# Optimization experiments

Hardware: AMD Instinct MI355X
Metric: run time of the kernel (lower is better)

## Reference

```python
import jax, jax.numpy as jnp
import numpy as np

B, L, O, K, H = 8192, 128, 512, 8, 20  # batch, num_latent, num_obs, causes/node, hidden


def setup_inputs() -> dict:
    key = jax.random.key(0)
    ks = jax.random.split(key, 7)
    x = jax.random.normal(ks[0], (B, L), dtype=jnp.float32)
    # noise ~ Normal(0, 0.1), one scalar per (sample, observed node); noise_coeff = 1.0
    noise = 0.1 * jax.random.normal(ks[1], (B, O), dtype=jnp.float32)
    # latent-cause indices per observed node (fixed in-degree K)
    cause_idx = jax.random.randint(ks[2], (O, K), 0, L, dtype=jnp.int32)
    # per-node MLP weights: Linear(K+1,H) -> tanh -> Linear(H,H) -> tanh -> Linear(H,1)
    W1 = jax.random.normal(ks[3], (O, K + 1, H), dtype=jnp.float32) / np.sqrt(K + 1).astype(np.float32)
    b1 = jnp.zeros((O, H), dtype=jnp.float32)
    W2 = jax.random.normal(ks[4], (O, H, H), dtype=jnp.float32) / np.sqrt(H).astype(np.float32)
    b2 = jnp.zeros((O, H), dtype=jnp.float32)
    W3 = jax.random.normal(ks[5], (O, H), dtype=jnp.float32) / np.sqrt(H).astype(np.float32)
    b3 = jnp.zeros((O,), dtype=jnp.float32)
    return {"x": x, "noise": noise, "cause_idx": cause_idx,
            "W1": W1, "b1": b1, "W2": W2, "b2": b2, "W3": W3, "b3": b3}


def reference(x, noise, cause_idx, W1, b1, W2, b2, W3, b3):
    # Gather each observed node's latent causes: [B, O, K]
    gathered = x[:, cause_idx]
    # Prepend the noise column (torch.cat((noise, x_subset), axis=1)): [B, O, K+1]
    inp = jnp.concatenate([noise[..., None], gathered], axis=-1)
    # Per-node tiny MLP as grouped batched GEMMs
    h = jnp.tanh(jnp.einsum('boi,oih->boh', inp, W1) + b1)   # [B, O, H]
    h = jnp.tanh(jnp.einsum('boh,ohg->bog', h, W2) + b2)     # [B, O, H]
    out = jnp.einsum('boh,oh->bo', h, W3) + b3               # [B, O] (concat of per-node outputs)
    return out
```

## Files before the change

kernel.cpp:

```cpp
#include <hip/hip_runtime.h>

#define B_TOT 8192
#define O_DIM 512
#define L_DIM 128
#define K_DIM 8
#define H_DIM 20

#define TB 64
#define G  16
#define NW 4
#define NTH 256
#define XSTR 65
#define NSTR 17

__device__ __forceinline__ float fast_tanh(float x) {
    float e = __builtin_amdgcn_exp2f(x * 2.885390081777927f);
    float r = __builtin_amdgcn_rcpf(1.0f + e);
    return 1.0f - 2.0f * r;
}

__global__ __launch_bounds__(NTH, 4) void medil_fused(
    const float* __restrict__ x, const float* __restrict__ noise,
    const int* __restrict__ cause_idx,
    const float* __restrict__ W1, const float* __restrict__ b1,
    const float* __restrict__ W2, const float* __restrict__ b2,
    const float* __restrict__ W3, const float* __restrict__ b3,
    float* __restrict__ out)
{
    __shared__ float xT[L_DIM * XSTR];
    __shared__ float nt[TB * NSTR];

    const int tid = threadIdx.x;
    const int o0 = (blockIdx.x & 31) * G;
    const int b0 = (blockIdx.x >> 5) * TB;

    {
        const float4* xg = (const float4*)(x + (size_t)b0 * L_DIM);
        #pragma unroll
        for (int i = 0; i < 8; ++i) {
            int idx = tid + NTH * i;
            int r = idx >> 5, c4 = idx & 31;
            float4 v = xg[r * 32 + c4];
            xT[(c4 * 4 + 0) * XSTR + r] = v.x;
            xT[(c4 * 4 + 1) * XSTR + r] = v.y;
            xT[(c4 * 4 + 2) * XSTR + r] = v.z;
            xT[(c4 * 4 + 3) * XSTR + r] = v.w;
        }
    }
    {
        int r = tid >> 2, c4 = tid & 3;
        float4 v = *(const float4*)(noise + (size_t)(b0 + r) * O_DIM + o0 + c4 * 4);
        nt[r * NSTR + c4 * 4 + 0] = v.x;
        nt[r * NSTR + c4 * 4 + 1] = v.y;
        nt[r * NSTR + c4 * 4 + 2] = v.z;
        nt[r * NSTR + c4 * 4 + 3] = v.w;
    }
    __syncthreads();

    const int lane = tid & 63;
    const int wv = tid >> 6;

    #pragma unroll
    for (int it = 0; it < G / NW; ++it) {
        const int ol = __builtin_amdgcn_readfirstlane(wv * (G / NW) + it);
        const int o  = o0 + ol;

        const float* w1p = W1 + (size_t)o * (K_DIM + 1) * H_DIM;
        const float* b1p = b1 + (size_t)o * H_DIM;
        const float* w2p = W2 + (size_t)o * H_DIM * H_DIM;
        const float* b2p = b2 + (size_t)o * H_DIM;
        const float* w3p = W3 + (size_t)o * H_DIM;
        const int*   cip = cause_idx + (size_t)o * K_DIM;

        float xi[K_DIM];
        #pragma unroll
        for (int k = 0; k < K_DIM; ++k)
            xi[k] = xT[cip[k] * XSTR + lane];
        float inp0 = nt[lane * NSTR + ol];

        float a1[H_DIM];
        #pragma unroll
        for (int h = 0; h < H_DIM; ++h)
            a1[h] = fmaf(inp0, w1p[h], b1p[h]);
        #pragma unroll
        for (int k = 0; k < K_DIM; ++k)
            #pragma unroll
            for (int h = 0; h < H_DIM; ++h)
                a1[h] = fmaf(xi[k], w1p[(k + 1) * H_DIM + h], a1[h]);
        #pragma unroll
        for (int h = 0; h < H_DIM; ++h) a1[h] = fast_tanh(a1[h]);

        float a2[H_DIM];
        #pragma unroll
        for (int g = 0; g < H_DIM; ++g) a2[g] = b2p[g];
        #pragma unroll
        for (int h = 0; h < H_DIM; ++h)
            #pragma unroll
            for (int g = 0; g < H_DIM; ++g)
                a2[g] = fmaf(a1[h], w2p[h * H_DIM + g], a2[g]);
        #pragma unroll
        for (int g = 0; g < H_DIM; ++g) a2[g] = fast_tanh(a2[g]);

        float r = b3[o];
        #pragma unroll
        for (int h = 0; h < H_DIM; ++h) r = fmaf(a2[h], w3p[h], r);
        out[(size_t)(b0 + lane) * O_DIM + o] = r;
    }
}

extern "C" void kernel_launch(void* const* d_in, const int* in_sizes, int n_in,
                              void* d_out, int out_size, void* d_ws, size_t ws_size,
                              hipStream_t stream) {
    const float* x         = (const float*)d_in[0];
    const float* noise     = (const float*)d_in[1];
    const int*   cause_idx = (const int*)d_in[2];
    const float* W1        = (const float*)d_in[3];
    const float* b1        = (const float*)d_in[4];
    const float* W2        = (const float*)d_in[5];
    const float* b2        = (const float*)d_in[6];
    const float* W3        = (const float*)d_in[7];
    const float* b3        = (const float*)d_in[8];
    float* out = (float*)d_out;

    dim3 grid((B_TOT / TB) * (O_DIM / G));
    dim3 block(NTH);
    hipLaunchKernelGGL(medil_fused, grid, block, 0, stream,
                       x, noise, cause_idx, W1, b1, W2, b2, W3, b3, out);
}
```

Baseline: 192.3 us.

## Use bf16 MFMA for hidden layer with smem-staged weights and bf16 latents

Replaces the per-lane scalar 20x20 second-layer GEMV with bf16 16x16x32 MFMA instructions. W2 is transposed and stored as bf16 in shared memory, W1 and the biases are staged in shared memory, and x is stored in shared memory as bf16 with an XOR swizzle. The tile becomes 8 output nodes per block, with each wave computing 8 hidden units per lane across four 16-row batch subtiles and reducing through shuffles. This aims to cut the FMA-bound VALU work and the global weight loads. The cost is bf16 rounding of the inputs and hidden activations, plus extra shared memory and lower occupancy.

```diff
diff --git a/kernel.cpp b/kernel.cpp
--- a/kernel.cpp
+++ b/kernel.cpp
@@ -1,4 +1,5 @@
 #include <hip/hip_runtime.h>
+#include <hip/hip_bf16.h>
 
 #define B_TOT 8192
 #define O_DIM 512
@@ -7,19 +8,31 @@
 #define H_DIM 20
 
 #define TB 64
-#define G  16
-#define NW 4
+#define TO 8
 #define NTH 256
-#define XSTR 65
-#define NSTR 17
+#define XPITCH 66
+
+typedef short bf16x8 __attribute__((ext_vector_type(8)));
+typedef float f32x4  __attribute__((ext_vector_type(4)));
+
+#define OFF_W2T 0
+#define OFF_W1  20480
+#define OFF_BB  29696
+#define OFF_NS  32768
+#define OFF_XT  35072
+#define SMEM_BYTES 51968
 
 __device__ __forceinline__ float fast_tanh(float x) {
     float e = __builtin_amdgcn_exp2f(x * 2.885390081777927f);
     float r = __builtin_amdgcn_rcpf(1.0f + e);
     return 1.0f - 2.0f * r;
 }
-
-__global__ __launch_bounds__(NTH, 4) void medil_fused(
+__device__ __forceinline__ unsigned short f2bf(float f) {
+    unsigned u = __float_as_uint(f);
+    return (unsigned short)((u + 0x8000u) >> 16);
+}
+
+__global__ __launch_bounds__(NTH, 3) void medil_fused(
     const float* __restrict__ x, const float* __restrict__ noise,
     const int* __restrict__ cause_idx,
     const float* __restrict__ W1, const float* __restrict__ b1,
@@ -27,84 +40,152 @@
     const float* __restrict__ W3, const float* __restrict__ b3,
     float* __restrict__ out)
 {
-    __shared__ float xT[L_DIM * XSTR];
-    __shared__ float nt[TB * NSTR];
+    __shared__ __align__(16) char smem[SMEM_BYTES];
+    unsigned short* w2t = (unsigned short*)(smem + OFF_W2T);
+    float*          w1s = (float*)(smem + OFF_W1);
+    float*          bbs = (float*)(smem + OFF_BB);
+    float*          nss = (float*)(smem + OFF_NS);
+    unsigned short* xts = (unsigned short*)(smem + OFF_XT);
 
     const int tid = threadIdx.x;
-    const int o0 = (blockIdx.x & 31) * G;
-    const int b0 = (blockIdx.x >> 5) * TB;
-
-    {
-        const float4* xg = (const float4*)(x + (size_t)b0 * L_DIM);
+    const int o0 = (blockIdx.x & 63) * TO;
+    const int b0 = (blockIdx.x >> 6) * TB;
+
+    {
+        const int ol = tid >> 5, idx = tid & 31;
+        unsigned int* w2z = (unsigned int*)(w2t + ol * 1280);
+        #pragma unroll
+        for (int z = 0; z < 20; ++z) w2z[idx + 32 * z] = 0u;
+        float* w1o = w1s + ol * 288;
+        #pragma unroll
+        for (int z = 0; z < 9; ++z) w1o[idx + 32 * z] = 0.f;
+        float* bbo = bbs + ol * 96;
+        #pragma unroll
+        for (int z = 0; z < 3; ++z) bbo[idx + 32 * z] = 0.f;
+    }
+    __syncthreads();
+    {
+        const int ol = tid >> 5, idx = tid & 31;
+        const int o = o0 + ol;
+        if (idx < 20) {
+            unsigned short* w2o = w2t + ol * 1280;
+            #pragma unroll
+            for (int hi = 0; hi < 20; ++hi)
+                w2o[idx * 40 + hi] = f2bf(W2[(size_t)o * 400 + hi * 20 + idx]);
+            float* w1o = w1s + ol * 288;
+            #pragma unroll
+            for (int k = 0; k < 9; ++k)
+                w1o[k * 32 + idx] = W1[(size_t)o * 180 + k * 20 + idx];
+            float* bbo = bbs + ol * 96;
+            bbo[idx]      = b1[o * H_DIM + idx];
+            bbo[32 + idx] = b2[o * H_DIM + idx];
+            bbo[64 + idx] = W3[o * H_DIM + idx];
+        }
+    }
+    {
+        const int r = tid >> 3, oln = tid & 7;
+        nss[r * 9 + oln]        = noise[(size_t)(b0 + r) * O_DIM + o0 + oln];
+        nss[(r + 32) * 9 + oln] = noise[(size_t)(b0 + r + 32) * O_DIM + o0 + oln];
+    }
+    {
         #pragma unroll
         for (int i = 0; i < 8; ++i) {
-            int idx = tid + NTH * i;
-            int r = idx >> 5, c4 = idx & 31;
-            float4 v = xg[r * 32 + c4];
-            xT[(c4 * 4 + 0) * XSTR + r] = v.x;
-            xT[(c4 * 4 + 1) * XSTR + r] = v.y;
-            xT[(c4 * 4 + 2) * XSTR + r] = v.z;
-            xT[(c4 * 4 + 3) * XSTR + r] = v.w;
-        }
-    }
-    {
-        int r = tid >> 2, c4 = tid & 3;
-        float4 v = *(const float4*)(noise + (size_t)(b0 + r) * O_DIM + o0 + c4 * 4);
-        nt[r * NSTR + c4 * 4 + 0] = v.x;
-        nt[r * NSTR + c4 * 4 + 1] = v.y;
-        nt[r * NSTR + c4 * 4 + 2] = v.z;
-        nt[r * NSTR + c4 * 4 + 3] = v.w;
+            int t = tid + NTH * i;
+            int c4 = t & 31, r = t >> 5;
+            float4 v = *(const float4*)(x + (size_t)(b0 + r) * L_DIM + 4 * c4);
+            float vv[4] = {v.x, v.y, v.z, v.w};
+            #pragma unroll
+            for (int s = 0; s < 4; ++s) {
+                int col = 4 * c4 + s;
+                xts[col * XPITCH + (r ^ (col & 31))] = f2bf(vv[s]);
+            }
+        }
     }
     __syncthreads();
 
     const int lane = tid & 63;
-    const int wv = tid >> 6;
-
-    #pragma unroll
-    for (int it = 0; it < G / NW; ++it) {
-        const int ol = __builtin_amdgcn_readfirstlane(wv * (G / NW) + it);
+    const int wv   = tid >> 6;
+    const int l15  = lane & 15;
+    const int q    = lane >> 4;
+
+    #pragma unroll 1
+    for (int oo = 0; oo < 2; ++oo) {
+        const int ol = __builtin_amdgcn_readfirstlane(2 * wv + oo);
         const int o  = o0 + ol;
 
-        const float* w1p = W1 + (size_t)o * (K_DIM + 1) * H_DIM;
-        const float* b1p = b1 + (size_t)o * H_DIM;
-        const float* w2p = W2 + (size_t)o * H_DIM * H_DIM;
-        const float* b2p = b2 + (size_t)o * H_DIM;
-        const float* w3p = W3 + (size_t)o * H_DIM;
-        const int*   cip = cause_idx + (size_t)o * K_DIM;
-
-        float xi[K_DIM];
-        #pragma unroll
-        for (int k = 0; k < K_DIM; ++k)
-            xi[k] = xT[cip[k] * XSTR + lane];
-        float inp0 = nt[lane * NSTR + ol];
-
-        float a1[H_DIM];
-        #pragma unroll
-        for (int h = 0; h < H_DIM; ++h)
-            a1[h] = fmaf(inp0, w1p[h], b1p[h]);
-        #pragma unroll
-        for (int k = 0; k < K_DIM; ++k)
-            #pragma unroll
-            for (int h = 0; h < H_DIM; ++h)
-                a1[h] = fmaf(xi[k], w1p[(k + 1) * H_DIM + h], a1[h]);
-        #pragma unroll
-        for (int h = 0; h < H_DIM; ++h) a1[h] = fast_tanh(a1[h]);
-
-        float a2[H_DIM];
-        #pragma unroll
-        for (int g = 0; g < H_DIM; ++g) a2[g] = b2p[g];
-        #pragma unroll
-        for (int h = 0; h < H_DIM; ++h)
-            #pragma unroll
-            for (int g = 0; g < H_DIM; ++g)
-                a2[g] = fmaf(a1[h], w2p[h * H_DIM + g], a2[g]);
-        #pragma unroll
-        for (int g = 0; g < H_DIM; ++g) a2[g] = fast_tanh(a2[g]);
-
-        float r = b3[o];
-        #pragma unroll
-        for (int h = 0; h < H_DIM; ++h) r = fmaf(a2[h], w3p[h], r);
-        out[(size_t)(b0 + lane) * O_DIM + o] = r;
+        float w1r[9][8];
+        const float* w1o = w1s + ol * 288;
+        #pragma unroll
+        for (int k = 0; k < 9; ++k) {
+            float4 lo = *(const float4*)(w1o + k * 32 + q * 8);
+            float4 hi = *(const float4*)(w1o + k * 32 + q * 8 + 4);
+            w1r[k][0] = lo.x; w1r[k][1] = lo.y; w1r[k][2] = lo.z; w1r[k][3] = lo.w;
+            w1r[k][4] = hi.x; w1r[k][5] = hi.y; w1r[k][6] = hi.z; w1r[k][7] = hi.w;
+        }
+        const float* bbo = bbs + ol * 96;
+        float b1r[8];
+        {
+            float4 lo = *(const float4*)(bbo + q * 8);
+            float4 hi = *(const float4*)(bbo + q * 8 + 4);
+            b1r[0] = lo.x; b1r[1] = lo.y; b1r[2] = lo.z; b1r[3] = lo.w;
+            b1r[4] = hi.x; b1r[5] = hi.y; b1r[6] = hi.z; b1r[7] = hi.w;
+        }
+        float4 b2a = *(const float4*)(bbo + 32 + 4 * q);
+        float4 b2b = *(const float4*)(bbo + 48 + 4 * q);
+        float4 w3a = *(const float4*)(bbo + 64 + 4 * q);
+        float4 w3b = *(const float4*)(bbo + 80 + 4 * q);
+        bf16x8 a2a = *(const bf16x8*)(w2t + ol * 1280 + l15 * 40 + q * 8);
+        bf16x8 a2b = *(const bf16x8*)(w2t + ol * 1280 + (16 + l15) * 40 + q * 8);
+        int cols[8];
+        {
+            const int* cip = cause_idx + o * K_DIM;
+            #pragma unroll
+            for (int k = 0; k < 8; ++k) cols[k] = cip[k];
+        }
+        const float b3v = b3[o];
+
+        #pragma unroll 1
+        for (int bt = 0; bt < 4; ++bt) {
+            const int row = bt * 16 + l15;
+            float nz = nss[row * 9 + ol];
+            float z[8];
+            #pragma unroll
+            for (int j = 0; j < 8; ++j) z[j] = fmaf(nz, w1r[0][j], b1r[j]);
+            #pragma unroll
+            for (int k = 0; k < 8; ++k) {
+                int col = cols[k];
+                unsigned short uh = xts[col * XPITCH + (row ^ (col & 31))];
+                float xv = __uint_as_float(((unsigned)uh) << 16);
+                #pragma unroll
+                for (int j = 0; j < 8; ++j) z[j] = fmaf(xv, w1r[k + 1][j], z[j]);
+            }
+            union { bf16x8 v; unsigned int u[4]; } b2v;
+            #pragma unroll
+            for (int i = 0; i < 4; ++i) {
+                float t0 = fast_tanh(z[2 * i]);
+                float t1 = fast_tanh(z[2 * i + 1]);
+                union { __hip_bfloat162 h; unsigned int u; } p;
+                p.h = __float22bfloat162_rn(make_float2(t0, t1));
+                b2v.u[i] = p.u;
+            }
+            f32x4 zero = {0.f, 0.f, 0.f, 0.f};
+            f32x4 c2a = __builtin_amdgcn_mfma_f32_16x16x32_bf16(a2a, b2v.v, zero, 0, 0, 0);
+            f32x4 c2b = __builtin_amdgcn_mfma_f32_16x16x32_bf16(a2b, b2v.v, zero, 0, 0, 0);
+            float s = 0.f;
+            s = fmaf(fast_tanh(c2a[0] + b2a.x), w3a.x, s);
+            s = fmaf(fast_tanh(c2a[1] + b2a.y), w3a.y, s);
+            s = fmaf(fast_tanh(c2a[2] + b2a.z), w3a.z, s);
+            s = fmaf(fast_tanh(c2a[3] + b2a.w), w3a.w, s);
+            s = fmaf(fast_tanh(c2b[0] + b2b.x), w3b.x, s);
+            s = fmaf(fast_tanh(c2b[1] + b2b.y), w3b.y, s);
+            s = fmaf(fast_tanh(c2b[2] + b2b.z), w3b.z, s);
+            s = fmaf(fast_tanh(c2b[3] + b2b.w), w3b.w, s);
+            s += __shfl_xor(s, 16);
+            s += __shfl_xor(s, 32);
+            s += b3v;
+            if (lane < 16)
+                out[(size_t)(b0 + row) * O_DIM + o] = s;
+        }
     }
 }
 
@@ -122,7 +203,7 @@
     const float* b3        = (const float*)d_in[8];
     float* out = (float*)d_out;
 
-    dim3 grid((B_TOT / TB) * (O_DIM / G));
+    dim3 grid((B_TOT / TB) * (O_DIM / TO));
     dim3 block(NTH);
     hipLaunchKernelGGL(medil_fused, grid, block, 0, stream,
                        x, noise, cause_idx, W1, b1, W2, b2, W3, b3, out);
```

Measured after the change: 201.2 us. 1.05x slower.
